# Performance work log

Hardware: AMD Instinct MI355X
Metric: run time of the kernel (lower is better)

The kernel has to match this reference:

```python
import jax, jax.numpy as jnp
import numpy as np

B, D, H1, H2, J, Q, O = 32768, 35, 256, 256, 12, 7, 5


def setup_inputs() -> dict:
    key = jax.random.key(0)
    ks = jax.random.split(key, 16)
    s = 0.05
    inp = {
        "x": jax.random.uniform(ks[0], (B, D), dtype=jnp.float32),
        "judge_ids": jax.random.randint(ks[1], (B,), 0, J, dtype=jnp.int32),
        # shared layers
        "W1_w": jax.random.normal(ks[2], (H1, D + 1), jnp.float32) * s,
        "W1_b": jnp.zeros((H1,), jnp.float32),
        "W2_w": jax.random.normal(ks[3], (H2, H1 + 1), jnp.float32) * s,
        "W2_b": jnp.zeros((H2,), jnp.float32),
        # judge-specific layers (stacked over J experts)
        "W1a_w": jax.random.normal(ks[4], (J, H1, D + 1), jnp.float32) * s,
        "W1a_b": jnp.zeros((J, H1), jnp.float32),
        "W2a_w": jax.random.normal(ks[5], (J, H2, H1 + 1), jnp.float32) * s,
        "W2a_b": jnp.zeros((J, H2), jnp.float32),
        # per-question output heads (shared + judge-specific)
        "V_w": jax.random.normal(ks[6], (Q, O, H2 + 1), jnp.float32) * s,
        "V_b": jnp.zeros((Q, O), jnp.float32),
        "Va_w": jax.random.normal(ks[7], (J, Q, O, H2 + 1), jnp.float32) * s,
        "Va_b": jnp.zeros((J, Q, O), jnp.float32),
    }
    return inp


def _append_ones(a):
    return jnp.concatenate([a, jnp.ones((a.shape[0], 1), a.dtype)], axis=1)


def reference(x, judge_ids, W1_w, W1_b, W2_w, W2_b, W1a_w, W1a_b, W2a_w, W2a_b, V_w, V_b, Va_w, Va_b):
    ids = judge_ids.astype(jnp.int32)
    xb = _append_ones(x)                                   # (B, D+1)
    # layer 1: shared + judge-routed
    a1 = jnp.einsum('bi,jhi->bjh', xb, W1a_w)              # (B, J, H1)
    j1 = jnp.take_along_axis(a1, ids[:, None, None], axis=1)[:, 0] + W1a_b[ids]
    z1 = jax.nn.relu(xb @ W1_w.T + W1_b + j1)              # (B, H1)
    z1b = _append_ones(z1)                                 # (B, H1+1)
    # layer 2
    a2 = jnp.einsum('bh,jgh->bjg', z1b, W2a_w)             # (B, J, H2)
    j2 = jnp.take_along_axis(a2, ids[:, None, None], axis=1)[:, 0] + W2a_b[ids]
    z2 = jax.nn.relu(z1b @ W2_w.T + W2_b + j2)             # (B, H2)
    z2b = _append_ones(z2)                                 # (B, H2+1)
    # per-question heads
    shared = jnp.einsum('bh,qoh->bqo', z2b, V_w) + V_b     # (B, Q, O)
    aV = jnp.einsum('bh,jqoh->bjqo', z2b, Va_w)            # (B, J, Q, O)
    jV = jnp.take_along_axis(aV, ids[:, None, None, None], axis=1)[:, 0] + Va_b[ids]
    return jax.nn.softmax(shared + jV, axis=-1)            # (B, Q, O)
```

## Files before the change

### kernel.cpp

```cpp
#include <hip/hip_runtime.h>
#include <stdint.h>

#define B_N   32768
#define D_IN  35
#define NJ    12
#define NQ    7
#define NO    5
#define QO    35
#define TILE  32
#define MAXSLOTS (B_N + NJ*TILE)
#define MAXT     (MAXSLOTS/TILE)

typedef __bf16  v8bf  __attribute__((ext_vector_type(8)));
typedef float   f32x4 __attribute__((ext_vector_type(4)));

__device__ __forceinline__ unsigned short f2bf(float f) {
    unsigned int u = __builtin_bit_cast(unsigned int, f);
    u += 0x7FFFu + ((u >> 16) & 1u);
    return (unsigned short)(u >> 16);
}
__device__ __forceinline__ unsigned int pack2(float a, float b) {
    return (unsigned int)f2bf(a) | ((unsigned int)f2bf(b) << 16);
}

__global__ void k_prep(const int* __restrict__ ids,
                       const float* __restrict__ W1_w, const float* __restrict__ W1_b,
                       const float* __restrict__ W2_w, const float* __restrict__ W2_b,
                       const float* __restrict__ W1a_w, const float* __restrict__ W1a_b,
                       const float* __restrict__ W2a_w, const float* __restrict__ W2a_b,
                       const float* __restrict__ V_w,  const float* __restrict__ V_b,
                       const float* __restrict__ Va_w, const float* __restrict__ Va_b,
                       unsigned short* __restrict__ w1c, unsigned short* __restrict__ w2c,
                       unsigned short* __restrict__ vc,
                       float* __restrict__ bias1, float* __restrict__ bias2,
                       float* __restrict__ biasv, int* __restrict__ counts)
{
    const int tid = blockIdx.x * blockDim.x + threadIdx.x;
    const int nth = gridDim.x * blockDim.x;

    for (int q = tid; q < NJ * 256 * 64; q += nth) {
        int k4 = (q & 63) << 2, h = (q >> 6) & 255, jj = q >> 14;
        const float* a = &W2_w[h * 257 + k4];
        const float* b = &W2a_w[(jj * 256 + h) * 257 + k4];
        ushort4 o;
        o.x = f2bf(a[0] + b[0]); o.y = f2bf(a[1] + b[1]);
        o.z = f2bf(a[2] + b[2]); o.w = f2bf(a[3] + b[3]);
        *(ushort4*)&w2c[(size_t)q << 2] = o;
    }
    for (int q = tid; q < NJ * 256 * 16; q += nth) {
        int k4 = (q & 15) << 2, h = (q >> 4) & 255, jj = q >> 12;
        ushort4 o;
        float v[4];
#pragma unroll
        for (int e = 0; e < 4; ++e) {
            int k = k4 + e;
            v[e] = (k < D_IN) ? (W1_w[h * 36 + k] + W1a_w[(jj * 256 + h) * 36 + k]) : 0.f;
        }
        o.x = f2bf(v[0]); o.y = f2bf(v[1]); o.z = f2bf(v[2]); o.w = f2bf(v[3]);
        *(ushort4*)&w1c[(size_t)q << 2] = o;
    }
    for (int q = tid; q < NJ * 48 * 64; q += nth) {
        int k4 = (q & 63) << 2, qo = (q >> 6) % 48, jj = q / (48 * 64);
        ushort4 o;
        if (qo < QO) {
            const float* a = &V_w[qo * 257 + k4];
            const float* b = &Va_w[(jj * QO + qo) * 257 + k4];
            o.x = f2bf(a[0] + b[0]); o.y = f2bf(a[1] + b[1]);
            o.z = f2bf(a[2] + b[2]); o.w = f2bf(a[3] + b[3]);
        } else {
            o.x = o.y = o.z = o.w = 0;
        }
        *(ushort4*)&vc[(size_t)q << 2] = o;
    }
    for (int i = tid; i < NJ * 256; i += nth) {
        int h = i & 255, jj = i >> 8;
        bias1[i] = W1_w[h * 36 + 35] + W1a_w[(jj * 256 + h) * 36 + 35] + W1_b[h] + W1a_b[i];
        bias2[i] = W2_w[h * 257 + 256] + W2a_w[(jj * 256 + h) * 257 + 256] + W2_b[h] + W2a_b[i];
    }
    for (int i = tid; i < NJ * 48; i += nth) {
        int qo = i % 48, jj = i / 48;
        float v = 0.f;
        if (qo < QO) v = V_w[qo * 257 + 256] + Va_w[(jj * QO + qo) * 257 + 256]
                       + V_b[qo] + Va_b[jj * QO + qo];
        biasv[i] = v;
    }
    __shared__ int lh[NJ];
    if (threadIdx.x < NJ) lh[threadIdx.x] = 0;
    __syncthreads();
    for (int i = tid; i < B_N; i += nth) atomicAdd(&lh[ids[i]], 1);
    __syncthreads();
    if (threadIdx.x < NJ && lh[threadIdx.x]) atomicAdd(&counts[threadIdx.x], lh[threadIdx.x]);
}

__global__ void k_scan(const int* __restrict__ counts, int* __restrict__ cursor,
                       int* __restrict__ ntiles, int* __restrict__ tileExpert)
{
    __shared__ int tb[NJ + 1];
    if (threadIdx.x == 0) {
        int off = 0, t = 0;
        for (int j = 0; j < NJ; ++j) {
            cursor[j] = off;
            tb[j] = t;
            int nt = (counts[j] + TILE - 1) / TILE;
            t += nt;
            off += nt * TILE;
        }
        tb[NJ] = t;
        ntiles[0] = t;
    }
    __syncthreads();
    int ntot = tb[NJ];
    for (int tt = threadIdx.x; tt < ntot; tt += blockDim.x) {
        int j = 0;
        while (tb[j + 1] <= tt) ++j;
        tileExpert[tt] = j;
    }
}

__global__ void k_scatter(const int* __restrict__ ids, int* __restrict__ cursor,
                          int* __restrict__ perm)
{
    __shared__ int lh[NJ], lbase[NJ];
    const int b = blockIdx.x * blockDim.x + threadIdx.x;
    if (threadIdx.x < NJ) lh[threadIdx.x] = 0;
    __syncthreads();
    int id = 0, rank = 0;
    if (b < B_N) { id = ids[b]; rank = atomicAdd(&lh[id], 1); }
    __syncthreads();
    if (threadIdx.x < NJ)
        lbase[threadIdx.x] = lh[threadIdx.x] ? atomicAdd(&cursor[threadIdx.x], lh[threadIdx.x]) : 0;
    __syncthreads();
    if (b < B_N) perm[lbase[id] + rank] = b;
}

__global__ __launch_bounds__(256, 4) void k_main(
    const float* __restrict__ x, float* __restrict__ out,
    const int* __restrict__ perm, const int* __restrict__ ntiles,
    const int* __restrict__ tileExpert,
    const unsigned short* __restrict__ w1c, const unsigned short* __restrict__ w2c,
    const unsigned short* __restrict__ vc,
    const float* __restrict__ bias1, const float* __restrict__ bias2,
    const float* __restrict__ biasv)
{
    __shared__ __align__(16) unsigned short s_z1[TILE][264];
    __shared__ __align__(16) union {
        unsigned short xb[TILE][72];
        float          lg[TILE][40];
    } s_u;
    __shared__ int s_rows[TILE];

    const int nt  = ntiles[0];
    const int bid = blockIdx.x;
    if (bid >= nt) return;

    const int q8 = nt >> 3, r8 = nt & 7;
    const int xcd = bid & 7, idx = bid >> 3;
    const int lbid = (xcd < r8 ? xcd * (q8 + 1) : r8 * (q8 + 1) + (xcd - r8) * q8) + idx;

    const int tid  = threadIdx.x;
    const int lane = tid & 63;
    const int wave = tid >> 6;
    const int l16  = lane & 15;
    const int lk   = lane >> 4;
    const int j    = tileExpert[lbid];

    if (tid < TILE) s_rows[tid] = perm[lbid * TILE + tid];
    for (int i = tid; i < TILE * 36; i += 256) ((unsigned int*)s_u.xb)[i] = 0u;
    __syncthreads();

    for (int i = tid; i < TILE * D_IN; i += 256) {
        int s = i / D_IN, k = i - s * D_IN;
        int r = s_rows[s];
        s_u.xb[s][k] = f2bf(r >= 0 ? x[(size_t)r * D_IN + k] : 0.f);
    }
    __syncthreads();

    const f32x4 vz = {0.f, 0.f, 0.f, 0.f};

    {
        v8bf b1[2][2];
#pragma unroll
        for (int mt = 0; mt < 2; ++mt) {
            b1[mt][0] = *(const v8bf*)&s_u.xb[mt * 16 + l16][lk * 8];
            b1[mt][1] = *(const v8bf*)&s_u.xb[mt * 16 + l16][32 + lk * 8];
        }
        const unsigned short* w1p = w1c + ((size_t)j << 14) + (size_t)(wave * 64) * 64;
        f32x4 acc[4][2];
#pragma unroll
        for (int t = 0; t < 4; ++t) { acc[t][0] = vz; acc[t][1] = vz; }
#pragma unroll
        for (int t = 0; t < 4; ++t) {
            const unsigned short* rp = w1p + (t * 16 + l16) * 64;
            v8bf a0 = *(const v8bf*)&rp[lk * 8];
            v8bf a1 = *(const v8bf*)&rp[32 + lk * 8];
#pragma unroll
            for (int mt = 0; mt < 2; ++mt) {
                acc[t][mt] = __builtin_amdgcn_mfma_f32_16x16x32_bf16(a0, b1[mt][0], acc[t][mt], 0, 0, 0);
                acc[t][mt] = __builtin_amdgcn_mfma_f32_16x16x32_bf16(a1, b1[mt][1], acc[t][mt], 0, 0, 0);
            }
        }
#pragma unroll
        for (int t = 0; t < 4; ++t) {
            f32x4 bz = *(const f32x4*)&bias1[j * 256 + wave * 64 + t * 16 + lk * 4];
#pragma unroll
            for (int mt = 0; mt < 2; ++mt) {
                float v0 = acc[t][mt][0] + bz[0], v1 = acc[t][mt][1] + bz[1];
                float v2 = acc[t][mt][2] + bz[2], v3 = acc[t][mt][3] + bz[3];
                v0 = v0 > 0.f ? v0 : 0.f; v1 = v1 > 0.f ? v1 : 0.f;
                v2 = v2 > 0.f ? v2 : 0.f; v3 = v3 > 0.f ? v3 : 0.f;
                uint2 pk; pk.x = pack2(v0, v1); pk.y = pack2(v2, v3);
                *(uint2*)&s_z1[mt * 16 + l16][wave * 64 + t * 16 + lk * 4] = pk;
            }
        }
    }
    __syncthreads();

    {
        f32x4 acc[4][2];
#pragma unroll
        for (int gt = 0; gt < 4; ++gt) { acc[gt][0] = vz; acc[gt][1] = vz; }
        const unsigned short* w2p = w2c + ((size_t)j << 16) + (size_t)(wave * 64) * 256;
#pragma unroll 2
        for (int hc = 0; hc < 8; ++hc) {
            v8bf bb0 = *(const v8bf*)&s_z1[l16][hc * 32 + lk * 8];
            v8bf bb1 = *(const v8bf*)&s_z1[16 + l16][hc * 32 + lk * 8];
#pragma unroll
            for (int gt = 0; gt < 4; ++gt) {
                v8bf a = *(const v8bf*)&w2p[(gt * 16 + l16) * 256 + hc * 32 + lk * 8];
                acc[gt][0] = __builtin_amdgcn_mfma_f32_16x16x32_bf16(a, bb0, acc[gt][0], 0, 0, 0);
                acc[gt][1] = __builtin_amdgcn_mfma_f32_16x16x32_bf16(a, bb1, acc[gt][1], 0, 0, 0);
            }
        }
        __syncthreads();
#pragma unroll
        for (int gt = 0; gt < 4; ++gt) {
            f32x4 bz = *(const f32x4*)&bias2[j * 256 + wave * 64 + gt * 16 + lk * 4];
#pragma unroll
            for (int mt = 0; mt < 2; ++mt) {
                float v0 = acc[gt][mt][0] + bz[0], v1 = acc[gt][mt][1] + bz[1];
                float v2 = acc[gt][mt][2] + bz[2], v3 = acc[gt][mt][3] + bz[3];
                v0 = v0 > 0.f ? v0 : 0.f; v1 = v1 > 0.f ? v1 : 0.f;
                v2 = v2 > 0.f ? v2 : 0.f; v3 = v3 > 0.f ? v3 : 0.f;
                uint2 pk; pk.x = pack2(v0, v1); pk.y = pack2(v2, v3);
                *(uint2*)&s_z1[mt * 16 + l16][wave * 64 + gt * 16 + lk * 4] = pk;
            }
        }
    }
    __syncthreads();

    if (wave < 3) {
        const unsigned short* vp = vc + (size_t)j * 12288 + (size_t)(wave * 16) * 256;
        f32x4 av[2] = {vz, vz};
#pragma unroll 2
        for (int gc = 0; gc < 8; ++gc) {
            v8bf bb0 = *(const v8bf*)&s_z1[l16][gc * 32 + lk * 8];
            v8bf bb1 = *(const v8bf*)&s_z1[16 + l16][gc * 32 + lk * 8];
            v8bf a = *(const v8bf*)&vp[l16 * 256 + gc * 32 + lk * 8];
            av[0] = __builtin_amdgcn_mfma_f32_16x16x32_bf16(a, bb0, av[0], 0, 0, 0);
            av[1] = __builtin_amdgcn_mfma_f32_16x16x32_bf16(a, bb1, av[1], 0, 0, 0);
        }
        int qb = wave * 16 + lk * 4;
        if (qb < 36) {
            f32x4 bz = *(const f32x4*)&biasv[j * 48 + qb];
#pragma unroll
            for (int mt = 0; mt < 2; ++mt) {
                f32x4 v = av[mt] + bz;
                *(f32x4*)&s_u.lg[mt * 16 + l16][qb] = v;
            }
        }
    }
    __syncthreads();

    if (tid < TILE * NQ) {
        int s = tid / NQ, qq = tid - s * NQ;
        int r = s_rows[s];
        if (r >= 0) {
            float l[NO], mx = -1e30f;
#pragma unroll
            for (int o = 0; o < NO; ++o) {
                l[o] = s_u.lg[s][qq * NO + o];
                mx = l[o] > mx ? l[o] : mx;
            }
            float sum = 0.f, e[NO];
#pragma unroll
            for (int o = 0; o < NO; ++o) { e[o] = __expf(l[o] - mx); sum += e[o]; }
            float inv = 1.f / sum;
            float* op = out + (size_t)r * QO + qq * NO;
#pragma unroll
            for (int o = 0; o < NO; ++o) op[o] = e[o] * inv;
        }
    }
}

extern "C" void kernel_launch(void* const* d_in, const int* in_sizes, int n_in,
                              void* d_out, int out_size, void* d_ws, size_t ws_size,
                              hipStream_t stream)
{
    const float* x     = (const float*)d_in[0];
    const int*   ids   = (const int*)d_in[1];
    const float* W1_w  = (const float*)d_in[2];
    const float* W1_b  = (const float*)d_in[3];
    const float* W2_w  = (const float*)d_in[4];
    const float* W2_b  = (const float*)d_in[5];
    const float* W1a_w = (const float*)d_in[6];
    const float* W1a_b = (const float*)d_in[7];
    const float* W2a_w = (const float*)d_in[8];
    const float* W2a_b = (const float*)d_in[9];
    const float* V_w   = (const float*)d_in[10];
    const float* V_b   = (const float*)d_in[11];
    const float* Va_w  = (const float*)d_in[12];
    const float* Va_b  = (const float*)d_in[13];
    float* out = (float*)d_out;

    char* ws = (char*)d_ws;
    size_t off = 0;
    auto take = [&](size_t nbytes) -> void* {
        void* p = ws + off;
        off = (off + nbytes + 255) & ~(size_t)255;
        return p;
    };
    unsigned short* w1c = (unsigned short*)take((size_t)NJ * 256 * 64 * 2);
    unsigned short* w2c = (unsigned short*)take((size_t)NJ * 256 * 256 * 2);
    unsigned short* vc  = (unsigned short*)take((size_t)NJ * 48 * 256 * 2);
    float* bias1        = (float*)take((size_t)NJ * 256 * 4);
    float* bias2        = (float*)take((size_t)NJ * 256 * 4);
    float* biasv        = (float*)take((size_t)NJ * 48 * 4);
    int* counts         = (int*)take(NJ * 4);
    int* cursor         = (int*)take(NJ * 4);
    int* ntiles         = (int*)take(4);
    int* tileExpert     = (int*)take(MAXT * 4);
    int* perm           = (int*)take((size_t)MAXSLOTS * 4);

    hipMemsetAsync(counts, 0, NJ * sizeof(int), stream);
    hipMemsetAsync(perm, 0xFF, (size_t)MAXSLOTS * sizeof(int), stream);

    k_prep<<<768, 256, 0, stream>>>(ids, W1_w, W1_b, W2_w, W2_b, W1a_w, W1a_b,
                                    W2a_w, W2a_b, V_w, V_b, Va_w, Va_b,
                                    w1c, w2c, vc, bias1, bias2, biasv, counts);
    k_scan<<<1, 256, 0, stream>>>(counts, cursor, ntiles, tileExpert);
    k_scatter<<<(B_N + 255) / 256, 256, 0, stream>>>(ids, cursor, perm);
    k_main<<<MAXT, 256, 0, stream>>>(x, out, perm, ntiles, tileExpert,
                                     w1c, w2c, vc, bias1, bias2, biasv);
}
```

Before: 55.42 us.

## Fold histogram and scan into prep kernel, drop memsets, prefetch weights early

Block 0 of the prep kernel now builds the expert histogram, the tile offsets and the tile-to-expert map. It also writes the -1 padding into perm. This removes the separate scan kernel and both memset launches. The main kernel loads the first layer-1, layer-2 and head weight fragments into registers before the barriers so global latency overlaps with shared-memory staging. This removes launch overhead and load stalls, at the cost of extra registers and a single-block serial histogram over the full batch.

```diff
diff --git a/kernel.cpp b/kernel.cpp
--- a/kernel.cpp
+++ b/kernel.cpp
@@ -33,7 +33,9 @@
                        unsigned short* __restrict__ w1c, unsigned short* __restrict__ w2c,
                        unsigned short* __restrict__ vc,
                        float* __restrict__ bias1, float* __restrict__ bias2,
-                       float* __restrict__ biasv, int* __restrict__ counts)
+                       float* __restrict__ biasv,
+                       int* __restrict__ cursor, int* __restrict__ ntiles,
+                       int* __restrict__ tileExpert, int* __restrict__ perm)
 {
     const int tid = blockIdx.x * blockDim.x + threadIdx.x;
     const int nth = gridDim.x * blockDim.x;
@@ -84,36 +86,46 @@
                        + V_b[qo] + Va_b[jj * QO + qo];
         biasv[i] = v;
     }
-    __shared__ int lh[NJ];
-    if (threadIdx.x < NJ) lh[threadIdx.x] = 0;
-    __syncthreads();
-    for (int i = tid; i < B_N; i += nth) atomicAdd(&lh[ids[i]], 1);
-    __syncthreads();
-    if (threadIdx.x < NJ && lh[threadIdx.x]) atomicAdd(&counts[threadIdx.x], lh[threadIdx.x]);
-}
-
-__global__ void k_scan(const int* __restrict__ counts, int* __restrict__ cursor,
-                       int* __restrict__ ntiles, int* __restrict__ tileExpert)
-{
-    __shared__ int tb[NJ + 1];
-    if (threadIdx.x == 0) {
-        int off = 0, t = 0;
-        for (int j = 0; j < NJ; ++j) {
-            cursor[j] = off;
-            tb[j] = t;
-            int nt = (counts[j] + TILE - 1) / TILE;
-            t += nt;
-            off += nt * TILE;
-        }
-        tb[NJ] = t;
-        ntiles[0] = t;
-    }
-    __syncthreads();
-    int ntot = tb[NJ];
-    for (int tt = threadIdx.x; tt < ntot; tt += blockDim.x) {
-        int j = 0;
-        while (tb[j + 1] <= tt) ++j;
-        tileExpert[tt] = j;
+
+    if (blockIdx.x == 0) {
+        __shared__ int lh[NJ];
+        __shared__ int s_cur[NJ], s_cnt[NJ], s_nt[NJ], tb[NJ + 1];
+        const int lt = threadIdx.x;
+        if (lt < NJ) lh[lt] = 0;
+        __syncthreads();
+        const int4* ids4 = (const int4*)ids;
+        for (int i = lt; i < B_N / 4; i += 256) {
+            int4 v = ids4[i];
+            atomicAdd(&lh[v.x], 1); atomicAdd(&lh[v.y], 1);
+            atomicAdd(&lh[v.z], 1); atomicAdd(&lh[v.w], 1);
+        }
+        __syncthreads();
+        if (lt == 0) {
+            int off = 0, t = 0;
+            for (int j = 0; j < NJ; ++j) {
+                int c = lh[j];
+                int nt = (c + TILE - 1) / TILE;
+                cursor[j] = off;
+                s_cur[j] = off; s_cnt[j] = c; s_nt[j] = nt; tb[j] = t;
+                t += nt;
+                off += nt * TILE;
+            }
+            tb[NJ] = t;
+            ntiles[0] = t;
+        }
+        __syncthreads();
+        const int ntot = tb[NJ];
+        for (int tt = lt; tt < ntot; tt += 256) {
+            int j = 0;
+            while (tb[j + 1] <= tt) ++j;
+            tileExpert[tt] = j;
+        }
+        for (int p = lt; p < NJ * TILE; p += 256) {
+            int j = p >> 5, o = p & 31;
+            int c = s_cnt[j];
+            int padN = s_nt[j] * TILE - c;
+            if (o < padN) perm[s_cur[j] + c + o] = -1;
+        }
     }
 }
 
@@ -164,6 +176,15 @@
     const int lk   = lane >> 4;
     const int j    = tileExpert[lbid];
 
+    const unsigned short* w1p = w1c + ((size_t)j << 14) + (size_t)(wave * 64) * 64;
+    v8bf w1a0[4], w1a1[4];
+#pragma unroll
+    for (int t = 0; t < 4; ++t) {
+        const unsigned short* rp = w1p + (t * 16 + l16) * 64;
+        w1a0[t] = *(const v8bf*)&rp[lk * 8];
+        w1a1[t] = *(const v8bf*)&rp[32 + lk * 8];
+    }
+
     if (tid < TILE) s_rows[tid] = perm[lbid * TILE + tid];
     for (int i = tid; i < TILE * 36; i += 256) ((unsigned int*)s_u.xb)[i] = 0u;
     __syncthreads();
@@ -184,21 +205,23 @@
             b1[mt][0] = *(const v8bf*)&s_u.xb[mt * 16 + l16][lk * 8];
             b1[mt][1] = *(const v8bf*)&s_u.xb[mt * 16 + l16][32 + lk * 8];
         }
-        const unsigned short* w1p = w1c + ((size_t)j << 14) + (size_t)(wave * 64) * 64;
         f32x4 acc[4][2];
 #pragma unroll
         for (int t = 0; t < 4; ++t) { acc[t][0] = vz; acc[t][1] = vz; }
 #pragma unroll
         for (int t = 0; t < 4; ++t) {
-            const unsigned short* rp = w1p + (t * 16 + l16) * 64;
-            v8bf a0 = *(const v8bf*)&rp[lk * 8];
-            v8bf a1 = *(const v8bf*)&rp[32 + lk * 8];
 #pragma unroll
             for (int mt = 0; mt < 2; ++mt) {
-                acc[t][mt] = __builtin_amdgcn_mfma_f32_16x16x32_bf16(a0, b1[mt][0], acc[t][mt], 0, 0, 0);
-                acc[t][mt] = __builtin_amdgcn_mfma_f32_16x16x32_bf16(a1, b1[mt][1], acc[t][mt], 0, 0, 0);
-            }
-        }
+                acc[t][mt] = __builtin_amdgcn_mfma_f32_16x16x32_bf16(w1a0[t], b1[mt][0], acc[t][mt], 0, 0, 0);
+                acc[t][mt] = __builtin_amdgcn_mfma_f32_16x16x32_bf16(w1a1[t], b1[mt][1], acc[t][mt], 0, 0, 0);
+            }
+        }
+        const unsigned short* w2p = w2c + ((size_t)j << 16) + (size_t)(wave * 64) * 256;
+        v8bf a2pre[4];
+#pragma unroll
+        for (int gt = 0; gt < 4; ++gt)
+            a2pre[gt] = *(const v8bf*)&w2p[(gt * 16 + l16) * 256 + lk * 8];
+
 #pragma unroll
         for (int t = 0; t < 4; ++t) {
             f32x4 bz = *(const f32x4*)&bias1[j * 256 + wave * 64 + t * 16 + lk * 4];
@@ -212,60 +235,75 @@
                 *(uint2*)&s_z1[mt * 16 + l16][wave * 64 + t * 16 + lk * 4] = pk;
             }
         }
-    }
-    __syncthreads();
-
-    {
-        f32x4 acc[4][2];
-#pragma unroll
-        for (int gt = 0; gt < 4; ++gt) { acc[gt][0] = vz; acc[gt][1] = vz; }
-        const unsigned short* w2p = w2c + ((size_t)j << 16) + (size_t)(wave * 64) * 256;
+        __syncthreads();
+
+        f32x4 acc2[4][2];
+#pragma unroll
+        for (int gt = 0; gt < 4; ++gt) { acc2[gt][0] = vz; acc2[gt][1] = vz; }
+        {
+            v8bf bb0 = *(const v8bf*)&s_z1[l16][lk * 8];
+            v8bf bb1 = *(const v8bf*)&s_z1[16 + l16][lk * 8];
+#pragma unroll
+            for (int gt = 0; gt < 4; ++gt) {
+                acc2[gt][0] = __builtin_amdgcn_mfma_f32_16x16x32_bf16(a2pre[gt], bb0, acc2[gt][0], 0, 0, 0);
+                acc2[gt][1] = __builtin_amdgcn_mfma_f32_16x16x32_bf16(a2pre[gt], bb1, acc2[gt][1], 0, 0, 0);
+            }
+        }
 #pragma unroll 2
-        for (int hc = 0; hc < 8; ++hc) {
+        for (int hc = 1; hc < 8; ++hc) {
             v8bf bb0 = *(const v8bf*)&s_z1[l16][hc * 32 + lk * 8];
             v8bf bb1 = *(const v8bf*)&s_z1[16 + l16][hc * 32 + lk * 8];
 #pragma unroll
             for (int gt = 0; gt < 4; ++gt) {
                 v8bf a = *(const v8bf*)&w2p[(gt * 16 + l16) * 256 + hc * 32 + lk * 8];
-                acc[gt][0] = __builtin_amdgcn_mfma_f32_16x16x32_bf16(a, bb0, acc[gt][0], 0, 0, 0);
-                acc[gt][1] = __builtin_amdgcn_mfma_f32_16x16x32_bf16(a, bb1, acc[gt][1], 0, 0, 0);
-            }
-        }
+                acc2[gt][0] = __builtin_amdgcn_mfma_f32_16x16x32_bf16(a, bb0, acc2[gt][0], 0, 0, 0);
+                acc2[gt][1] = __builtin_amdgcn_mfma_f32_16x16x32_bf16(a, bb1, acc2[gt][1], 0, 0, 0);
+            }
+        }
+        const unsigned short* vp = vc + (size_t)j * 12288 + (size_t)(wave * 16) * 256;
+        v8bf a3pre;
+        if (wave < 3) a3pre = *(const v8bf*)&vp[l16 * 256 + lk * 8];
+
         __syncthreads();
 #pragma unroll
         for (int gt = 0; gt < 4; ++gt) {
             f32x4 bz = *(const f32x4*)&bias2[j * 256 + wave * 64 + gt * 16 + lk * 4];
 #pragma unroll
             for (int mt = 0; mt < 2; ++mt) {
-                float v0 = acc[gt][mt][0] + bz[0], v1 = acc[gt][mt][1] + bz[1];
-                float v2 = acc[gt][mt][2] + bz[2], v3 = acc[gt][mt][3] + bz[3];
+                float v0 = acc2[gt][mt][0] + bz[0], v1 = acc2[gt][mt][1] + bz[1];
+                float v2 = acc2[gt][mt][2] + bz[2], v3 = acc2[gt][mt][3] + bz[3];
                 v0 = v0 > 0.f ? v0 : 0.f; v1 = v1 > 0.f ? v1 : 0.f;
                 v2 = v2 > 0.f ? v2 : 0.f; v3 = v3 > 0.f ? v3 : 0.f;
                 uint2 pk; pk.x = pack2(v0, v1); pk.y = pack2(v2, v3);
                 *(uint2*)&s_z1[mt * 16 + l16][wave * 64 + gt * 16 + lk * 4] = pk;
             }
         }
-    }
-    __syncthreads();
-
-    if (wave < 3) {
-        const unsigned short* vp = vc + (size_t)j * 12288 + (size_t)(wave * 16) * 256;
-        f32x4 av[2] = {vz, vz};
-#pragma unroll 2
-        for (int gc = 0; gc < 8; ++gc) {
-            v8bf bb0 = *(const v8bf*)&s_z1[l16][gc * 32 + lk * 8];
-            v8bf bb1 = *(const v8bf*)&s_z1[16 + l16][gc * 32 + lk * 8];
-            v8bf a = *(const v8bf*)&vp[l16 * 256 + gc * 32 + lk * 8];
-            av[0] = __builtin_amdgcn_mfma_f32_16x16x32_bf16(a, bb0, av[0], 0, 0, 0);
-            av[1] = __builtin_amdgcn_mfma_f32_16x16x32_bf16(a, bb1, av[1], 0, 0, 0);
-        }
-        int qb = wave * 16 + lk * 4;
-        if (qb < 36) {
-            f32x4 bz = *(const f32x4*)&biasv[j * 48 + qb];
-#pragma unroll
-            for (int mt = 0; mt < 2; ++mt) {
-                f32x4 v = av[mt] + bz;
-                *(f32x4*)&s_u.lg[mt * 16 + l16][qb] = v;
+        __syncthreads();
+
+        if (wave < 3) {
+            f32x4 av[2] = {vz, vz};
+            {
+                v8bf bb0 = *(const v8bf*)&s_z1[l16][lk * 8];
+                v8bf bb1 = *(const v8bf*)&s_z1[16 + l16][lk * 8];
+                av[0] = __builtin_amdgcn_mfma_f32_16x16x32_bf16(a3pre, bb0, av[0], 0, 0, 0);
+                av[1] = __builtin_amdgcn_mfma_f32_16x16x32_bf16(a3pre, bb1, av[1], 0, 0, 0);
+            }
+#pragma unroll 4
+            for (int gc = 1; gc < 8; ++gc) {
+                v8bf bb0 = *(const v8bf*)&s_z1[l16][gc * 32 + lk * 8];
+                v8bf bb1 = *(const v8bf*)&s_z1[16 + l16][gc * 32 + lk * 8];
+                v8bf a = *(const v8bf*)&vp[l16 * 256 + gc * 32 + lk * 8];
+                av[0] = __builtin_amdgcn_mfma_f32_16x16x32_bf16(a, bb0, av[0], 0, 0, 0);
+                av[1] = __builtin_amdgcn_mfma_f32_16x16x32_bf16(a, bb1, av[1], 0, 0, 0);
+            }
+            int qb = wave * 16 + lk * 4;
+            if (qb < 36) {
+                f32x4 bz = *(const f32x4*)&biasv[j * 48 + qb];
+#pragma unroll
+                for (int mt = 0; mt < 2; ++mt) {
+                    f32x4 v = av[mt] + bz;
+                    *(f32x4*)&s_u.lg[mt * 16 + l16][qb] = v;
+                }
             }
         }
     }
@@ -325,19 +363,15 @@
     float* bias1        = (float*)take((size_t)NJ * 256 * 4);
     float* bias2        = (float*)take((size_t)NJ * 256 * 4);
     float* biasv        = (float*)take((size_t)NJ * 48 * 4);
-    int* counts         = (int*)take(NJ * 4);
     int* cursor         = (int*)take(NJ * 4);
     int* ntiles         = (int*)take(4);
     int* tileExpert     = (int*)take(MAXT * 4);
     int* perm           = (int*)take((size_t)MAXSLOTS * 4);
 
-    hipMemsetAsync(counts, 0, NJ * sizeof(int), stream);
-    hipMemsetAsync(perm, 0xFF, (size_t)MAXSLOTS * sizeof(int), stream);
-
     k_prep<<<768, 256, 0, stream>>>(ids, W1_w, W1_b, W2_w, W2_b, W1a_w, W1a_b,
                                     W2a_w, W2a_b, V_w, V_b, Va_w, Va_b,
-                                    w1c, w2c, vc, bias1, bias2, biasv, counts);
-    k_scan<<<1, 256, 0, stream>>>(counts, cursor, ntiles, tileExpert);
+                                    w1c, w2c, vc, bias1, bias2, biasv,
+                                    cursor, ntiles, tileExpert, perm);
     k_scatter<<<(B_N + 255) / 256, 256, 0, stream>>>(ids, cursor, perm);
     k_main<<<MAXT, 256, 0, stream>>>(x, out, perm, ntiles, tileExpert,
                                      w1c, w2c, vc, bias1, bias2, biasv);
```

Result: faster. 51.49 us (-7.1%).
